# Optimization experiments

Measured on AMD Instinct MI355X. Metric: run time of the kernel, lower is better.

Reference implementation:

```python
import jax, jax.numpy as jnp
import numpy as np

DIM = 768
HEADS = 12
HEAD_DIM = DIM // HEADS
SCALE = HEAD_DIM ** -0.5


def setup_inputs() -> dict:
    key = jax.random.key(0)
    ks = jax.random.split(key, 7)
    B, N, C = 4, 1024, DIM
    s = 0.02
    return {
        "x": jax.random.normal(ks[0], (B, N, C), dtype=jnp.float32),
        "attn_mask": jax.random.normal(ks[1], (B, N, N), dtype=jnp.float32) * 0.1,
        "w_qkv": jax.random.normal(ks[2], (3 * C, C), dtype=jnp.float32) * s,
        "w_proj": jax.random.normal(ks[3], (C, C), dtype=jnp.float32) * s,
        "b_proj": jnp.zeros((C,), dtype=jnp.float32),
        "w_pre": jax.random.normal(ks[4], (HEADS, HEADS), dtype=jnp.float32) * 0.2,
        "w_post": jax.random.normal(ks[5], (HEADS, HEADS), dtype=jnp.float32) * 0.2,
    }


def reference(x, attn_mask, w_qkv, w_proj, b_proj, w_pre, w_post):
    B, N, C = x.shape
    H, D = HEADS, HEAD_DIM
    qkv = (x @ w_qkv.T).reshape(B, N, 3, H, D)
    q, k, v = jnp.moveaxis(qkv, 2, 0)          # each [B, N, H, D]
    q = q.transpose(0, 2, 1, 3)                # [B, H, N, D]
    k = k.transpose(0, 2, 1, 3)
    v = v.transpose(0, 2, 1, 3)
    attn = jnp.einsum("bhnd,bhmd->bhnm", q, k) * SCALE
    attn = attn + attn_mask[:, None, :, :]
    # talking-heads pre-softmax mixing: Linear over head axis (y = x @ W.T)
    attn = jnp.einsum("bhnm,gh->bgnm", attn, w_pre)
    attn = jax.nn.softmax(attn, axis=-1)
    # talking-heads post-softmax mixing
    attn = jnp.einsum("bhnm,gh->bgnm", attn, w_post)
    out = jnp.einsum("bhnm,bhmd->bhnd", attn, v)   # [B, H, N, D]
    out = out.transpose(0, 2, 1, 3).reshape(B, N, C)
    return out @ w_proj.T + b_proj
```

## Files before the change

kernel.cpp:

```cpp
#include <hip/hip_runtime.h>
#include <hip/hip_bf16.h>

typedef __attribute__((ext_vector_type(8))) short bf16x8;
typedef __attribute__((ext_vector_type(4))) float f32x4;
typedef unsigned short u16;
typedef unsigned int u32;

#define ATT_SCALE 0.125f

__device__ __forceinline__ u16 f2bf(float f){
  __hip_bfloat16 h = __float2bfloat16(f);
  return *reinterpret_cast<u16*>(&h);
}
__device__ __forceinline__ float bf2f(u16 u){
  __hip_bfloat16 h;
  *reinterpret_cast<u16*>(&h) = u;
  return __bfloat162float(h);
}

__global__ __launch_bounds__(256) void cvt_kernel(const float* __restrict__ src,
                                                  u16* __restrict__ dst, int n4){
  int i = blockIdx.x*256 + threadIdx.x;
  if (i < n4){
    float4 v = reinterpret_cast<const float4*>(src)[i];
    ushort4 o;
    o.x = f2bf(v.x); o.y = f2bf(v.y); o.z = f2bf(v.z); o.w = f2bf(v.w);
    reinterpret_cast<ushort4*>(dst)[i] = o;
  }
}

template<int BM, int BN, int MODE>
__global__ __launch_bounds__(256) void gemm_bt(
    const u16* __restrict__ A, const u16* __restrict__ B,
    void* __restrict__ C0, void* __restrict__ C1, void* __restrict__ C2,
    const float* __restrict__ bias,
    int M, int N, int K, int lda, int ldb, long sA, long sB, long sC)
{
  constexpr int BK = 32, LDT = 40;
  __shared__ u16 As[BM*LDT];
  __shared__ u16 Bs[BN*LDT];
  const int z = blockIdx.z;
  const u16* Ab = A + (long)z * sA;
  const u16* Bb = B + (long)z * sB;
  const int bm = blockIdx.x * BM, bn = blockIdx.y * BN;
  const int tid = threadIdx.x, lane = tid & 63, wv = tid >> 6;
  constexpr int WM = BM/2, WN = BN/2, FM = WM/16, FN = WN/16;
  const int wm = (wv >> 1) * WM, wn = (wv & 1) * WN;
  const int quad = lane >> 4, cl = lane & 15;
  f32x4 acc[FM][FN];
  #pragma unroll
  for (int i=0;i<FM;i++)
    #pragma unroll
    for (int j=0;j<FN;j++){ f32x4 zr = {0.f,0.f,0.f,0.f}; acc[i][j] = zr; }
  constexpr int AIT = (BM*BK)/(8*256);
  constexpr int BIT = (BN*BK)/(8*256);

  for (int kb = 0; kb < K; kb += BK){
    __syncthreads();
    #pragma unroll
    for (int sL=0; sL<AIT; sL++){
      int e = tid + sL*256, r = e >> 2, c8 = (e & 3) * 8;
      *reinterpret_cast<float4*>(&As[r*LDT + c8]) =
        *reinterpret_cast<const float4*>(Ab + (long)(bm + r)*lda + kb + c8);
    }
    #pragma unroll
    for (int sL=0; sL<BIT; sL++){
      int e = tid + sL*256, r = e >> 2, c8 = (e & 3) * 8;
      *reinterpret_cast<float4*>(&Bs[r*LDT + c8]) =
        *reinterpret_cast<const float4*>(Bb + (long)(bn + r)*ldb + kb + c8);
    }
    __syncthreads();
    bf16x8 af[FM], bfr[FN];
    #pragma unroll
    for (int i=0;i<FM;i++)
      af[i] = *reinterpret_cast<const bf16x8*>(&As[(wm + i*16 + cl)*LDT + quad*8]);
    #pragma unroll
    for (int j=0;j<FN;j++)
      bfr[j] = *reinterpret_cast<const bf16x8*>(&Bs[(wn + j*16 + cl)*LDT + quad*8]);
    #pragma unroll
    for (int i=0;i<FM;i++)
      #pragma unroll
      for (int j=0;j<FN;j++)
        acc[i][j] = __builtin_amdgcn_mfma_f32_16x16x32_bf16(af[i], bfr[j], acc[i][j], 0, 0, 0);
  }

  #pragma unroll
  for (int i=0;i<FM;i++)
  #pragma unroll
  for (int j=0;j<FN;j++)
  #pragma unroll
  for (int r=0;r<4;r++){
    int gm = bm + wm + i*16 + quad*4 + r;
    int gn = bn + wn + j*16 + cl;
    float v = acc[i][j][r];
    if (MODE == 0){
      int b_ = gm >> 10, n_ = gm & 1023;
      int t3 = (gn >= 1536) ? 2 : ((gn >= 768) ? 1 : 0);
      int rem = gn - t3*768;
      int h = rem >> 6, d = rem & 63;
      u16 hv = f2bf(v);
      if (t3 == 0)      ((u16*)C0)[((long)((b_*12 + h)*1024 + n_))*64 + d] = hv;
      else if (t3 == 1) ((u16*)C1)[((long)((b_*12 + h)*1024 + n_))*64 + d] = hv;
      else              ((u16*)C2)[((long)((b_*12 + h)*64 + d))*1024 + n_] = hv;
    } else if (MODE == 1){
      ((u16*)C0)[(long)z*sC + (long)gm*N + gn] = f2bf(v);
    } else if (MODE == 2){
      int b_ = z / 12, h = z - b_*12;
      ((u16*)C0)[((long)((b_*1024 + gm)*12 + h))*64 + gn] = f2bf(v);
    } else {
      ((float*)C0)[(long)gm*N + gn] = v + bias[gn];
    }
  }
}

#define SMP 1032

__global__ __launch_bounds__(256) void mix2_kernel(
    u16* __restrict__ S, const float* __restrict__ mask,
    const float* __restrict__ w_pre, const float* __restrict__ w_post)
{
  __shared__ u16 Sh[12*SMP];
  __shared__ float maskS[1024];
  __shared__ float Lred[4][16];
  __shared__ float LinvS[16];

  const int bid = blockIdx.x;
  const int b = bid >> 10, n = bid & 1023;
  const int t = threadIdx.x, wv = t >> 6, lane = t & 63;
  const int quad = lane >> 4, cl = lane & 15;

  #pragma unroll
  for (int it = 0; it < 6; it++){
    int idx = t + it*256;
    int h = idx >> 7, m = (idx & 127)*8;
    *reinterpret_cast<float4*>(&Sh[h*SMP + m]) =
      *reinterpret_cast<const float4*>(S + ((long)((b*12 + h)*1024 + n))*1024 + m);
  }
  for (int i = t; i < 1024; i += 256)
    maskS[i] = mask[((long)(b*1024 + n))*1024 + i];

  float rs_[4];
  #pragma unroll
  for (int r = 0; r < 4; r++){
    int g = quad*4 + r;
    float v = 0.f;
    if (g < 12)
      for (int h = 0; h < 12; h++) v += w_pre[g*12 + h];
    rs_[r] = v;
  }
  union FragU { bf16x8 v; u32 u[4]; u16 s[8]; };
  FragU a_pre;
  #pragma unroll
  for (int j = 0; j < 8; j++){
    int k = quad*8 + j;
    a_pre.s[j] = (cl < 12 && k < 12) ? f2bf(w_pre[cl*12 + k] * ATT_SCALE) : (u16)0;
  }
  __syncthreads();

  u32 Ep01[16], Ep23[16];
  float Lacc[4] = {0.f, 0.f, 0.f, 0.f};
  const f32x4 zero4 = {0.f, 0.f, 0.f, 0.f};

  #pragma unroll
  for (int j = 0; j < 16; j++){
    int mcol = (wv*16 + j)*16 + cl;
    FragU bs;
    #pragma unroll
    for (int jj = 0; jj < 8; jj++){
      int hh = quad*8 + jj;
      bs.s[jj] = (hh < 12) ? Sh[hh*SMP + mcol] : (u16)0;
    }
    f32x4 d = __builtin_amdgcn_mfma_f32_16x16x32_bf16(a_pre.v, bs.v, zero4, 0, 0, 0);
    float mval = maskS[mcol];
    float e0 = __expf(d[0] + rs_[0]*mval);
    float e1 = __expf(d[1] + rs_[1]*mval);
    float e2 = __expf(d[2] + rs_[2]*mval);
    float e3 = __expf(d[3] + rs_[3]*mval);
    Lacc[0] += e0; Lacc[1] += e1; Lacc[2] += e2; Lacc[3] += e3;
    Ep01[j] = (u32)f2bf(e0) | ((u32)f2bf(e1) << 16);
    Ep23[j] = (u32)f2bf(e2) | ((u32)f2bf(e3) << 16);
  }

  #pragma unroll
  for (int r = 0; r < 4; r++){
    float v = Lacc[r];
    v += __shfl_xor(v, 1); v += __shfl_xor(v, 2);
    v += __shfl_xor(v, 4); v += __shfl_xor(v, 8);
    Lacc[r] = v;
  }
  if (cl == 0){
    #pragma unroll
    for (int r = 0; r < 4; r++) Lred[wv][quad*4 + r] = Lacc[r];
  }
  __syncthreads();
  if (t < 16) LinvS[t] = 1.f / (Lred[0][t] + Lred[1][t] + Lred[2][t] + Lred[3][t]);
  __syncthreads();

  FragU a_post;
  #pragma unroll
  for (int j = 0; j < 8; j++){
    int k = quad*8 + j;
    a_post.s[j] = (cl < 12 && k < 12) ? f2bf(w_post[cl*12 + k] * LinvS[k]) : (u16)0;
  }

  const int srcA = (quad << 5) + cl;
  #pragma unroll
  for (int j = 0; j < 16; j++){
    int mcol = (wv*16 + j)*16 + cl;
    FragU be;
    be.u[0] = (u32)__shfl((int)Ep01[j], srcA, 64);
    be.u[1] = (u32)__shfl((int)Ep23[j], srcA, 64);
    be.u[2] = (u32)__shfl((int)Ep01[j], srcA + 16, 64);
    be.u[3] = (u32)__shfl((int)Ep23[j], srcA + 16, 64);
    f32x4 d = __builtin_amdgcn_mfma_f32_16x16x32_bf16(a_post.v, be.v, zero4, 0, 0, 0);
    if (quad < 3){
      #pragma unroll
      for (int r = 0; r < 4; r++){
        int h = quad*4 + r;
        S[((long)((b*12 + h)*1024 + n))*1024 + mcol] = f2bf(d[r]);
      }
    }
  }
}

extern "C" void kernel_launch(void* const* d_in, const int* in_sizes, int n_in,
                              void* d_out, int out_size, void* d_ws, size_t ws_size,
                              hipStream_t stream)
{
  const float* x      = (const float*)d_in[0];
  const float* mask   = (const float*)d_in[1];
  const float* w_qkv  = (const float*)d_in[2];
  const float* w_proj = (const float*)d_in[3];
  const float* b_proj = (const float*)d_in[4];
  const float* w_pre  = (const float*)d_in[5];
  const float* w_post = (const float*)d_in[6];
  float* out = (float*)d_out;

  u16* xb     = (u16*)d_ws;
  u16* wqkvb  = xb     + 4096l*768;
  u16* wprojb = wqkvb  + 2304l*768;
  u16* Qb     = wprojb + 768l*768;
  u16* Kb     = Qb     + 48l*1024*64;
  u16* Vtb    = Kb     + 48l*1024*64;
  u16* tmpb   = Vtb    + 48l*1024*64;
  u16* Sb     = tmpb   + 4096l*768;
  size_t need = ((size_t)(Sb - xb) + 48ul*1024*1024) * sizeof(u16);
  if (ws_size < need) return;

  cvt_kernel<<<(4096*768/4 + 255)/256, 256, 0, stream>>>(x,      xb,     4096*768/4);
  cvt_kernel<<<(2304*768/4 + 255)/256, 256, 0, stream>>>(w_qkv,  wqkvb,  2304*768/4);
  cvt_kernel<<<(768*768/4  + 255)/256, 256, 0, stream>>>(w_proj, wprojb, 768*768/4);

  dim3 gq(4096/128, 2304/128, 1);
  gemm_bt<128,128,0><<<gq, 256, 0, stream>>>(xb, wqkvb, Qb, Kb, Vtb, nullptr,
      4096, 2304, 768, 768, 768, 0, 0, 0);

  dim3 gs(1024/128, 1024/128, 48);
  gemm_bt<128,128,1><<<gs, 256, 0, stream>>>(Qb, Kb, Sb, nullptr, nullptr, nullptr,
      1024, 1024, 64, 64, 64, 1024l*64, 1024l*64, 1024l*1024);

  mix2_kernel<<<4096, 256, 0, stream>>>(Sb, mask, w_pre, w_post);

  dim3 gp(1024/128, 1, 48);
  gemm_bt<128,64,2><<<gp, 256, 0, stream>>>(Sb, Vtb, tmpb, nullptr, nullptr, nullptr,
      1024, 64, 1024, 1024, 1024, 1024l*1024, 64l*1024, 0);

  dim3 go(4096/128, 768/128, 1);
  gemm_bt<128,128,3><<<go, 256, 0, stream>>>(tmpb, wprojb, out, nullptr, nullptr, b_proj,
      4096, 768, 768, 768, 768, 0, 0, 0);
}
```

Measured before the change: 281.5 us.

## Transpose score slab to head-minor layout in mix kernel and tune GEMM K-tiles

The mixing kernel now stores scores in shared memory in a position-major, head-minor slab, so each lane gathers its MFMA B operand with two 64-bit reads instead of eight scalar reads. The softmax numerators are written back into the same slab, which replaces the cross-lane shuffles. exp is switched to exp2 with log2e folded into the weights. The GEMM gains a BK template parameter (64 for the QK and PV GEMMs), and the output projection uses narrower 64-column tiles for more blocks. The costs are a strided, uncoalesced-to-LDS global gather of S and a larger shared footprint of about 56KB, which lowers occupancy.

New measurement: 280.5 us. Within noise of the previous version (-0.4%).

```diff
diff --git a/kernel.cpp b/kernel.cpp
--- a/kernel.cpp
+++ b/kernel.cpp
@@ -5,17 +5,13 @@
 typedef __attribute__((ext_vector_type(4))) float f32x4;
 typedef unsigned short u16;
 typedef unsigned int u32;
+typedef unsigned long long u64;
 
 #define ATT_SCALE 0.125f
 
 __device__ __forceinline__ u16 f2bf(float f){
   __hip_bfloat16 h = __float2bfloat16(f);
   return *reinterpret_cast<u16*>(&h);
-}
-__device__ __forceinline__ float bf2f(u16 u){
-  __hip_bfloat16 h;
-  *reinterpret_cast<u16*>(&h) = u;
-  return __bfloat162float(h);
 }
 
 __global__ __launch_bounds__(256) void cvt_kernel(const float* __restrict__ src,
@@ -29,14 +25,14 @@
   }
 }
 
-template<int BM, int BN, int MODE>
+template<int BM, int BN, int BK, int MODE>
 __global__ __launch_bounds__(256) void gemm_bt(
     const u16* __restrict__ A, const u16* __restrict__ B,
     void* __restrict__ C0, void* __restrict__ C1, void* __restrict__ C2,
     const float* __restrict__ bias,
     int M, int N, int K, int lda, int ldb, long sA, long sB, long sC)
 {
-  constexpr int BK = 32, LDT = 40;
+  constexpr int LDT = BK + 8;
   __shared__ u16 As[BM*LDT];
   __shared__ u16 Bs[BN*LDT];
   const int z = blockIdx.z;
@@ -52,6 +48,7 @@
   for (int i=0;i<FM;i++)
     #pragma unroll
     for (int j=0;j<FN;j++){ f32x4 zr = {0.f,0.f,0.f,0.f}; acc[i][j] = zr; }
+  constexpr int KV = BK/8;
   constexpr int AIT = (BM*BK)/(8*256);
   constexpr int BIT = (BN*BK)/(8*256);
 
@@ -59,29 +56,32 @@
     __syncthreads();
     #pragma unroll
     for (int sL=0; sL<AIT; sL++){
-      int e = tid + sL*256, r = e >> 2, c8 = (e & 3) * 8;
+      int e = tid + sL*256, r = e / KV, c8 = (e % KV) * 8;
       *reinterpret_cast<float4*>(&As[r*LDT + c8]) =
         *reinterpret_cast<const float4*>(Ab + (long)(bm + r)*lda + kb + c8);
     }
     #pragma unroll
     for (int sL=0; sL<BIT; sL++){
-      int e = tid + sL*256, r = e >> 2, c8 = (e & 3) * 8;
+      int e = tid + sL*256, r = e / KV, c8 = (e % KV) * 8;
       *reinterpret_cast<float4*>(&Bs[r*LDT + c8]) =
         *reinterpret_cast<const float4*>(Bb + (long)(bn + r)*ldb + kb + c8);
     }
     __syncthreads();
-    bf16x8 af[FM], bfr[FN];
-    #pragma unroll
-    for (int i=0;i<FM;i++)
-      af[i] = *reinterpret_cast<const bf16x8*>(&As[(wm + i*16 + cl)*LDT + quad*8]);
-    #pragma unroll
-    for (int j=0;j<FN;j++)
-      bfr[j] = *reinterpret_cast<const bf16x8*>(&Bs[(wn + j*16 + cl)*LDT + quad*8]);
-    #pragma unroll
-    for (int i=0;i<FM;i++)
+    #pragma unroll
+    for (int kk=0; kk<BK; kk+=32){
+      bf16x8 af[FM], bfr[FN];
+      #pragma unroll
+      for (int i=0;i<FM;i++)
+        af[i] = *reinterpret_cast<const bf16x8*>(&As[(wm + i*16 + cl)*LDT + kk + quad*8]);
       #pragma unroll
       for (int j=0;j<FN;j++)
-        acc[i][j] = __builtin_amdgcn_mfma_f32_16x16x32_bf16(af[i], bfr[j], acc[i][j], 0, 0, 0);
+        bfr[j] = *reinterpret_cast<const bf16x8*>(&Bs[(wn + j*16 + cl)*LDT + kk + quad*8]);
+      #pragma unroll
+      for (int i=0;i<FM;i++)
+        #pragma unroll
+        for (int j=0;j<FN;j++)
+          acc[i][j] = __builtin_amdgcn_mfma_f32_16x16x32_bf16(af[i], bfr[j], acc[i][j], 0, 0, 0);
+    }
   }
 
   #pragma unroll
@@ -113,32 +113,45 @@
   }
 }
 
-#define SMP 1032
-
-__global__ __launch_bounds__(256) void mix2_kernel(
+__global__ __launch_bounds__(256) void mix3_kernel(
     u16* __restrict__ S, const float* __restrict__ mask,
     const float* __restrict__ w_pre, const float* __restrict__ w_post)
 {
-  __shared__ u16 Sh[12*SMP];
+  __shared__ u16 slab[1024*28];
   __shared__ float maskS[1024];
   __shared__ float Lred[4][16];
-  __shared__ float LinvS[16];
+  __shared__ float invLs[16];
 
   const int bid = blockIdx.x;
   const int b = bid >> 10, n = bid & 1023;
   const int t = threadIdx.x, wv = t >> 6, lane = t & 63;
   const int quad = lane >> 4, cl = lane & 15;
-
-  #pragma unroll
-  for (int it = 0; it < 6; it++){
-    int idx = t + it*256;
-    int h = idx >> 7, m = (idx & 127)*8;
-    *reinterpret_cast<float4*>(&Sh[h*SMP + m]) =
-      *reinterpret_cast<const float4*>(S + ((long)((b*12 + h)*1024 + n))*1024 + m);
-  }
-  for (int i = t; i < 1024; i += 256)
-    maskS[i] = mask[((long)(b*1024 + n))*1024 + i];
-
+  const float LOG2E = 1.4426950408889634f;
+
+  #pragma unroll
+  for (int h = 0; h < 12; h++){
+    const u16* Srow = S + ((long)((b*12 + h)*1024 + n))*1024;
+    #pragma unroll
+    for (int p = 0; p < 4; p++){
+      int m = t + p*256;
+      slab[m*28 + h] = Srow[m];
+    }
+  }
+  #pragma unroll
+  for (int p = 0; p < 4; p++){
+    int m = t + p*256;
+    *reinterpret_cast<u64*>(&slab[m*28 + 12]) = 0ull;
+  }
+  *reinterpret_cast<float4*>(&maskS[t*4]) =
+      *reinterpret_cast<const float4*>(mask + ((long)(b*1024 + n))*1024 + t*4);
+
+  union FragU { bf16x8 v; u64 d[2]; u16 s[8]; };
+  FragU a_pre;
+  #pragma unroll
+  for (int j = 0; j < 8; j++){
+    int k = quad*8 + j;
+    a_pre.s[j] = (cl < 12 && k < 12) ? f2bf(w_pre[cl*12 + k] * (ATT_SCALE*LOG2E)) : (u16)0;
+  }
   float rs_[4];
   #pragma unroll
   for (int r = 0; r < 4; r++){
@@ -146,39 +159,29 @@
     float v = 0.f;
     if (g < 12)
       for (int h = 0; h < 12; h++) v += w_pre[g*12 + h];
-    rs_[r] = v;
-  }
-  union FragU { bf16x8 v; u32 u[4]; u16 s[8]; };
-  FragU a_pre;
-  #pragma unroll
-  for (int j = 0; j < 8; j++){
-    int k = quad*8 + j;
-    a_pre.s[j] = (cl < 12 && k < 12) ? f2bf(w_pre[cl*12 + k] * ATT_SCALE) : (u16)0;
+    rs_[r] = v * LOG2E;
   }
   __syncthreads();
 
-  u32 Ep01[16], Ep23[16];
-  float Lacc[4] = {0.f, 0.f, 0.f, 0.f};
-  const f32x4 zero4 = {0.f, 0.f, 0.f, 0.f};
-
+  const f32x4 z4 = {0.f,0.f,0.f,0.f};
+  float Lacc[4] = {0.f,0.f,0.f,0.f};
+  const bool qlo = (quad < 2);
   #pragma unroll
   for (int j = 0; j < 16; j++){
-    int mcol = (wv*16 + j)*16 + cl;
+    int mcol = wv*256 + j*16 + cl;
     FragU bs;
-    #pragma unroll
-    for (int jj = 0; jj < 8; jj++){
-      int hh = quad*8 + jj;
-      bs.s[jj] = (hh < 12) ? Sh[hh*SMP + mcol] : (u16)0;
-    }
-    f32x4 d = __builtin_amdgcn_mfma_f32_16x16x32_bf16(a_pre.v, bs.v, zero4, 0, 0, 0);
-    float mval = maskS[mcol];
-    float e0 = __expf(d[0] + rs_[0]*mval);
-    float e1 = __expf(d[1] + rs_[1]*mval);
-    float e2 = __expf(d[2] + rs_[2]*mval);
-    float e3 = __expf(d[3] + rs_[3]*mval);
+    bs.d[0] = qlo ? *reinterpret_cast<const u64*>(&slab[mcol*28 + quad*8])     : 0ull;
+    bs.d[1] = qlo ? *reinterpret_cast<const u64*>(&slab[mcol*28 + quad*8 + 4]) : 0ull;
+    f32x4 d = __builtin_amdgcn_mfma_f32_16x16x32_bf16(a_pre.v, bs.v, z4, 0, 0, 0);
+    float mv = maskS[mcol];
+    float e0 = exp2f(d[0] + rs_[0]*mv);
+    float e1 = exp2f(d[1] + rs_[1]*mv);
+    float e2 = exp2f(d[2] + rs_[2]*mv);
+    float e3 = exp2f(d[3] + rs_[3]*mv);
     Lacc[0] += e0; Lacc[1] += e1; Lacc[2] += e2; Lacc[3] += e3;
-    Ep01[j] = (u32)f2bf(e0) | ((u32)f2bf(e1) << 16);
-    Ep23[j] = (u32)f2bf(e2) | ((u32)f2bf(e3) << 16);
+    u64 pk = (u64)f2bf(e0) | ((u64)f2bf(e1) << 16)
+           | ((u64)f2bf(e2) << 32) | ((u64)f2bf(e3) << 48);
+    *reinterpret_cast<u64*>(&slab[mcol*28 + quad*4]) = pk;
   }
 
   #pragma unroll
@@ -193,26 +196,23 @@
     for (int r = 0; r < 4; r++) Lred[wv][quad*4 + r] = Lacc[r];
   }
   __syncthreads();
-  if (t < 16) LinvS[t] = 1.f / (Lred[0][t] + Lred[1][t] + Lred[2][t] + Lred[3][t]);
+  if (t < 16) invLs[t] = 1.f / (Lred[0][t] + Lred[1][t] + Lred[2][t] + Lred[3][t]);
   __syncthreads();
 
   FragU a_post;
   #pragma unroll
   for (int j = 0; j < 8; j++){
     int k = quad*8 + j;
-    a_post.s[j] = (cl < 12 && k < 12) ? f2bf(w_post[cl*12 + k] * LinvS[k]) : (u16)0;
-  }
-
-  const int srcA = (quad << 5) + cl;
+    a_post.s[j] = (cl < 12 && k < 12) ? f2bf(w_post[cl*12 + k] * invLs[k]) : (u16)0;
+  }
+
   #pragma unroll
   for (int j = 0; j < 16; j++){
-    int mcol = (wv*16 + j)*16 + cl;
+    int mcol = wv*256 + j*16 + cl;
     FragU be;
-    be.u[0] = (u32)__shfl((int)Ep01[j], srcA, 64);
-    be.u[1] = (u32)__shfl((int)Ep23[j], srcA, 64);
-    be.u[2] = (u32)__shfl((int)Ep01[j], srcA + 16, 64);
-    be.u[3] = (u32)__shfl((int)Ep23[j], srcA + 16, 64);
-    f32x4 d = __builtin_amdgcn_mfma_f32_16x16x32_bf16(a_post.v, be.v, zero4, 0, 0, 0);
+    be.d[0] = qlo ? *reinterpret_cast<const u64*>(&slab[mcol*28 + quad*8])     : 0ull;
+    be.d[1] = qlo ? *reinterpret_cast<const u64*>(&slab[mcol*28 + quad*8 + 4]) : 0ull;
+    f32x4 d = __builtin_amdgcn_mfma_f32_16x16x32_bf16(a_post.v, be.v, z4, 0, 0, 0);
     if (quad < 3){
       #pragma unroll
       for (int r = 0; r < 4; r++){
@@ -252,20 +252,20 @@
   cvt_kernel<<<(768*768/4  + 255)/256, 256, 0, stream>>>(w_proj, wprojb, 768*768/4);
 
   dim3 gq(4096/128, 2304/128, 1);
-  gemm_bt<128,128,0><<<gq, 256, 0, stream>>>(xb, wqkvb, Qb, Kb, Vtb, nullptr,
+  gemm_bt<128,128,32,0><<<gq, 256, 0, stream>>>(xb, wqkvb, Qb, Kb, Vtb, nullptr,
       4096, 2304, 768, 768, 768, 0, 0, 0);
 
   dim3 gs(1024/128, 1024/128, 48);
-  gemm_bt<128,128,1><<<gs, 256, 0, stream>>>(Qb, Kb, Sb, nullptr, nullptr, nullptr,
+  gemm_bt<128,128,64,1><<<gs, 256, 0, stream>>>(Qb, Kb, Sb, nullptr, nullptr, nullptr,
       1024, 1024, 64, 64, 64, 1024l*64, 1024l*64, 1024l*1024);
 
-  mix2_kernel<<<4096, 256, 0, stream>>>(Sb, mask, w_pre, w_post);
+  mix3_kernel<<<4096, 256, 0, stream>>>(Sb, mask, w_pre, w_post);
 
   dim3 gp(1024/128, 1, 48);
-  gemm_bt<128,64,2><<<gp, 256, 0, stream>>>(Sb, Vtb, tmpb, nullptr, nullptr, nullptr,
+  gemm_bt<128,64,64,2><<<gp, 256, 0, stream>>>(Sb, Vtb, tmpb, nullptr, nullptr, nullptr,
       1024, 64, 1024, 1024, 1024, 1024l*1024, 64l*1024, 0);
 
-  dim3 go(4096/128, 768/128, 1);
-  gemm_bt<128,128,3><<<go, 256, 0, stream>>>(tmpb, wprojb, out, nullptr, nullptr, b_proj,
+  dim3 go(4096/128, 768/64, 1);
+  gemm_bt<128,64,32,3><<<go, 256, 0, stream>>>(tmpb, wprojb, out, nullptr, nullptr, b_proj,
       4096, 768, 768, 768, 768, 0, 0, 0);
 }
```
